# Kernel tuning notes

Hardware: AMD Instinct MI355X
Metric: run time of the kernel (lower is better)

## Reference

```python
import jax, jax.numpy as jnp
import numpy as np

NUM_ENTS = 1000
NUM_RELS = 100
HIDDEN = 200
N_QUERY = 50000
N_HIST = 1000000
ALPHA = 0.5


def setup_inputs() -> dict:
    key = jax.random.key(0)
    ks = jax.random.split(key, 12)
    s = 0.05  # small init for numerical stability (xavier-like scale)
    return {
        "ent_emb": jax.random.normal(ks[0], (NUM_ENTS, HIDDEN), jnp.float32) * s,
        "rel_emb": jax.random.normal(ks[1], (NUM_RELS, HIDDEN), jnp.float32) * s,
        "tim_emb": jax.random.normal(ks[2], (1, HIDDEN), jnp.float32) * s,
        "g_w": jax.random.normal(ks[3], (3 * HIDDEN, HIDDEN), jnp.float32) * s,
        "g_b": jnp.zeros((HIDDEN,), jnp.float32),
        "c_w": jax.random.normal(ks[4], (3 * HIDDEN, HIDDEN), jnp.float32) * s,
        "c_b": jnp.zeros((HIDDEN,), jnp.float32),
        "hist_sub": jax.random.randint(ks[5], (N_HIST,), 0, NUM_ENTS, jnp.int32),
        "hist_rel": jax.random.randint(ks[6], (N_HIST,), 0, NUM_RELS, jnp.int32),
        "hist_obj": jax.random.randint(ks[7], (N_HIST,), 0, NUM_ENTS, jnp.int32),
        "sub": jax.random.randint(ks[8], (N_QUERY,), 0, NUM_ENTS, jnp.int32),
        "rel": jax.random.randint(ks[9], (N_QUERY,), 0, NUM_RELS, jnp.int32),
    }


def reference(ent_emb, rel_emb, tim_emb, g_w, g_b, c_w, c_b,
              hist_sub, hist_rel, hist_obj, sub, rel):
    E = ent_emb.shape[0]
    R = rel_emb.shape[0]
    N = sub.shape[0]
    # Triple-count histogram over all history graphs (fused scatter-add;
    # equivalent to the per-graph python loop vocab[s,r,o] += 1).
    vocab = jnp.zeros((E, R, E), jnp.float32).at[hist_sub, hist_rel, hist_obj].add(1.0)
    # Query features: [N, 3H]
    x = jnp.concatenate(
        [ent_emb[sub], rel_emb[rel], jnp.broadcast_to(tim_emb, (N, tim_emb.shape[1]))],
        axis=1)
    # Generate-mode score distribution
    gscore = jax.nn.softmax(x @ g_w + g_b, axis=1)  # [N, H]
    # Copy-mode mask: 1 where the (sub, rel) pair occurred in history
    mask = (vocab[sub, rel].sum(axis=1, keepdims=True) != 0).astype(x.dtype)  # [N, 1]
    cscore = jax.nn.softmax(jnp.tanh(x @ c_w + c_b) + mask, axis=1)  # [N, H]
    fscore = gscore + ALPHA * (cscore - gscore)
    return jnp.log(fscore)
```

## Files before the change

kernel.cpp:

```cpp
#include <hip/hip_runtime.h>
#include <math.h>

#define HIDDEN 200
#define RPB 8

#define LOG2E 1.4426950408889634f
#define LN2   0.6931471805599453f

typedef float f32x4 __attribute__((ext_vector_type(4)));

__global__ __launch_bounds__(256) void precompute_kernel(
    const float* __restrict__ ent, const float* __restrict__ rel,
    const float* __restrict__ tim,
    const float* __restrict__ g_w, const float* __restrict__ g_b,
    const float* __restrict__ c_w, const float* __restrict__ c_b,
    float* __restrict__ Ag, float* __restrict__ Ac,
    float* __restrict__ Bg, float* __restrict__ Bc) {
  const float* in;
  const float* w;
  const float* bias = nullptr;
  float* out;
  int nrows, k0;
  bool fold_tim = false;
  switch (blockIdx.y) {
    case 0:  in = ent; w = g_w; out = Ag; nrows = 1000; k0 = 0;   break;
    case 1:  in = ent; w = c_w; out = Ac; nrows = 1000; k0 = 0;   break;
    case 2:  in = rel; w = g_w; out = Bg; nrows = 100;  k0 = 200;
             fold_tim = true; bias = g_b; break;
    default: in = rel; w = c_w; out = Bc; nrows = 100;  k0 = 200;
             fold_tim = true; bias = c_b; break;
  }
  int row0 = blockIdx.x * RPB;
  if (row0 >= nrows) return;
  int nr = nrows - row0;
  if (nr > RPB) nr = RPB;

  __shared__ float a_lds[RPB][HIDDEN];
  __shared__ float t_lds[HIDDEN];
  int c = threadIdx.x;
  if (c < HIDDEN) {
    for (int j = 0; j < nr; ++j) a_lds[j][c] = in[(row0 + j) * HIDDEN + c];
    if (fold_tim) t_lds[c] = tim[c];
  }
  __syncthreads();
  if (c >= HIDDEN) return;

  float acc[RPB];
  #pragma unroll
  for (int j = 0; j < RPB; ++j) acc[j] = 0.f;
  const float* wp = w + k0 * HIDDEN + c;
  #pragma unroll 4
  for (int k = 0; k < HIDDEN; ++k) {
    float wv = wp[k * HIDDEN];
    #pragma unroll
    for (int j = 0; j < RPB; ++j) acc[j] += a_lds[j][k] * wv;
  }
  float extra = 0.f;
  if (fold_tim) {
    const float* wt = w + 400 * HIDDEN + c;
    float t = 0.f;
    #pragma unroll 4
    for (int k = 0; k < HIDDEN; ++k) t += t_lds[k] * wt[k * HIDDEN];
    extra = t + bias[c];
  }
  for (int j = 0; j < nr; ++j) out[(row0 + j) * HIDDEN + c] = acc[j] + extra;
}

__global__ __launch_bounds__(256) void query_kernel(
    const float* __restrict__ Ag, const float* __restrict__ Ac,
    const float* __restrict__ Bg, const float* __restrict__ Bc,
    const int* __restrict__ sub, const int* __restrict__ rel,
    float* __restrict__ out, int N) {
  int gtid = blockIdx.x * blockDim.x + threadIdx.x;
  int q = gtid >> 6;
  int lane = threadIdx.x & 63;
  if (q >= N) return;

  int s = __builtin_amdgcn_readfirstlane(sub[q]);
  int r = __builtin_amdgcn_readfirstlane(rel[q]);
  bool act = lane < (HIDDEN / 4);

  float eg[4], ec[4];
  float sg = 0.f, sc = 0.f;
  if (act) {
    float4 a = ((const float4*)(Ag + s * HIDDEN))[lane];
    float4 b = ((const float4*)(Bg + r * HIDDEN))[lane];
    float lg0 = a.x + b.x, lg1 = a.y + b.y, lg2 = a.z + b.z, lg3 = a.w + b.w;
    eg[0] = __builtin_amdgcn_exp2f(lg0 * LOG2E);
    eg[1] = __builtin_amdgcn_exp2f(lg1 * LOG2E);
    eg[2] = __builtin_amdgcn_exp2f(lg2 * LOG2E);
    eg[3] = __builtin_amdgcn_exp2f(lg3 * LOG2E);
    sg = (eg[0] + eg[1]) + (eg[2] + eg[3]);

    a = ((const float4*)(Ac + s * HIDDEN))[lane];
    b = ((const float4*)(Bc + r * HIDDEN))[lane];
    float xc[4] = {a.x + b.x, a.y + b.y, a.z + b.z, a.w + b.w};
    #pragma unroll
    for (int j = 0; j < 4; ++j) {
      float x = fminf(fmaxf(xc[j], -10.f), 10.f);
      float e2 = __builtin_amdgcn_exp2f(x * (2.f * LOG2E));
      float th = (e2 - 1.f) * __builtin_amdgcn_rcpf(e2 + 1.f);
      ec[j] = __builtin_amdgcn_exp2f(th * LOG2E);
      sc += ec[j];
    }
  }
  #pragma unroll
  for (int m = 32; m > 0; m >>= 1) {
    sg += __shfl_xor(sg, m);
    sc += __shfl_xor(sc, m);
  }

  if (act) {
    float ig = 0.5f * __builtin_amdgcn_rcpf(sg);
    float ic = 0.5f * __builtin_amdgcn_rcpf(sc);
    f32x4 o;
    o.x = __builtin_amdgcn_logf(eg[0] * ig + ec[0] * ic) * LN2;
    o.y = __builtin_amdgcn_logf(eg[1] * ig + ec[1] * ic) * LN2;
    o.z = __builtin_amdgcn_logf(eg[2] * ig + ec[2] * ic) * LN2;
    o.w = __builtin_amdgcn_logf(eg[3] * ig + ec[3] * ic) * LN2;
    __builtin_nontemporal_store(o, (f32x4*)(out + q * HIDDEN) + lane);
  }
}

extern "C" void kernel_launch(void* const* d_in, const int* in_sizes, int n_in,
                              void* d_out, int out_size, void* d_ws, size_t ws_size,
                              hipStream_t stream) {
  const float* ent  = (const float*)d_in[0];
  const float* relE = (const float*)d_in[1];
  const float* tim  = (const float*)d_in[2];
  const float* g_w  = (const float*)d_in[3];
  const float* g_b  = (const float*)d_in[4];
  const float* c_w  = (const float*)d_in[5];
  const float* c_b  = (const float*)d_in[6];
  const int* sub = (const int*)d_in[10];
  const int* rel = (const int*)d_in[11];
  float* out = (float*)d_out;
  int N = in_sizes[10];

  float* ws = (float*)d_ws;
  float* Ag = ws;
  float* Ac = ws + 200000;
  float* Bg = ws + 400000;
  float* Bc = ws + 420000;

  dim3 grid1((1000 + RPB - 1) / RPB, 4);
  precompute_kernel<<<grid1, 256, 0, stream>>>(ent, relE, tim, g_w, g_b, c_w,
                                               c_b, Ag, Ac, Bg, Bc);

  long long threads = (long long)N * 64;
  int blocks = (int)((threads + 255) / 256);
  query_kernel<<<blocks, 256, 0, stream>>>(Ag, Ac, Bg, Bc, sub, rel, out, N);
}
```

Before: 138.9 us.

## Precompute exponentiated gen logits, interleave tables, and factor the log-sum

The precompute kernel now stores exp of the generate-mode partial logits, so the query kernel gets the softmax numerator as a product of entity and relation terms instead of an add followed by exp. The g and c tables are interleaved per row so one query reads a single contiguous 400-float row for the entity and one for the relation. The final log is rewritten as log(eg*sc+ec*sg) minus a shared log(2*sg*sc), which replaces the two reciprocals and per-element scaling. The precompute grid is restructured to two rows per block with split accumulators. The tanh input clamp is removed, which risks inf/NaN for large inputs, and exp products without max subtraction could overflow for larger weights.

Measured after the change: 125.2 us, median of 2. 9.8% less time.

```diff
diff --git a/kernel.cpp b/kernel.cpp
--- a/kernel.cpp
+++ b/kernel.cpp
@@ -2,8 +2,6 @@
 #include <math.h>
 
 #define HIDDEN 200
-#define RPB 8
-
 #define LOG2E 1.4426950408889634f
 #define LN2   0.6931471805599453f
 
@@ -14,61 +12,62 @@
     const float* __restrict__ tim,
     const float* __restrict__ g_w, const float* __restrict__ g_b,
     const float* __restrict__ c_w, const float* __restrict__ c_b,
-    float* __restrict__ Ag, float* __restrict__ Ac,
-    float* __restrict__ Bg, float* __restrict__ Bc) {
-  const float* in;
-  const float* w;
-  const float* bias = nullptr;
-  float* out;
-  int nrows, k0;
-  bool fold_tim = false;
-  switch (blockIdx.y) {
-    case 0:  in = ent; w = g_w; out = Ag; nrows = 1000; k0 = 0;   break;
-    case 1:  in = ent; w = c_w; out = Ac; nrows = 1000; k0 = 0;   break;
-    case 2:  in = rel; w = g_w; out = Bg; nrows = 100;  k0 = 200;
-             fold_tim = true; bias = g_b; break;
-    default: in = rel; w = c_w; out = Bc; nrows = 100;  k0 = 200;
-             fold_tim = true; bias = c_b; break;
-  }
-  int row0 = blockIdx.x * RPB;
-  if (row0 >= nrows) return;
-  int nr = nrows - row0;
-  if (nr > RPB) nr = RPB;
+    float* __restrict__ EA, float* __restrict__ EB) {
+  const int mode = blockIdx.y;
+  const float* w = mode ? c_w : g_w;
+  const float* bias = mode ? c_b : g_b;
+  const bool is_ent = blockIdx.x < 500;
+  const int row0 = is_ent ? blockIdx.x * 2 : (blockIdx.x - 500) * 2;
+  const float* in = is_ent ? ent : rel;
+  const int k0 = is_ent ? 0 : 200;
+  float* obase = is_ent ? (EA + row0 * 400 + mode * 200)
+                        : (EB + row0 * 400 + mode * 200);
 
-  __shared__ float a_lds[RPB][HIDDEN];
-  __shared__ float t_lds[HIDDEN];
-  int c = threadIdx.x;
+  __shared__ float a0[HIDDEN], a1[HIDDEN], tl[HIDDEN];
+  const int c = threadIdx.x;
   if (c < HIDDEN) {
-    for (int j = 0; j < nr; ++j) a_lds[j][c] = in[(row0 + j) * HIDDEN + c];
-    if (fold_tim) t_lds[c] = tim[c];
+    a0[c] = in[row0 * HIDDEN + c];
+    a1[c] = in[(row0 + 1) * HIDDEN + c];
+    if (!is_ent) tl[c] = tim[c];
   }
   __syncthreads();
   if (c >= HIDDEN) return;
 
-  float acc[RPB];
-  #pragma unroll
-  for (int j = 0; j < RPB; ++j) acc[j] = 0.f;
   const float* wp = w + k0 * HIDDEN + c;
+  float acc0a = 0.f, acc0b = 0.f, acc1a = 0.f, acc1b = 0.f;
   #pragma unroll 4
-  for (int k = 0; k < HIDDEN; ++k) {
-    float wv = wp[k * HIDDEN];
-    #pragma unroll
-    for (int j = 0; j < RPB; ++j) acc[j] += a_lds[j][k] * wv;
+  for (int k = 0; k < 100; ++k) {
+    float w0 = wp[k * HIDDEN];
+    float w1 = wp[(k + 100) * HIDDEN];
+    acc0a += a0[k] * w0;
+    acc0b += a0[k + 100] * w1;
+    acc1a += a1[k] * w0;
+    acc1b += a1[k + 100] * w1;
   }
-  float extra = 0.f;
-  if (fold_tim) {
+  float r0 = acc0a + acc0b;
+  float r1 = acc1a + acc1b;
+  if (!is_ent) {
     const float* wt = w + 400 * HIDDEN + c;
-    float t = 0.f;
+    float ta = 0.f, tb = 0.f;
     #pragma unroll 4
-    for (int k = 0; k < HIDDEN; ++k) t += t_lds[k] * wt[k * HIDDEN];
-    extra = t + bias[c];
+    for (int k = 0; k < 100; ++k) {
+      ta += tl[k] * wt[k * HIDDEN];
+      tb += tl[k + 100] * wt[(k + 100) * HIDDEN];
+    }
+    float extra = ta + tb + bias[c];
+    r0 += extra;
+    r1 += extra;
   }
-  for (int j = 0; j < nr; ++j) out[(row0 + j) * HIDDEN + c] = acc[j] + extra;
+  if (mode == 0) {
+    r0 = __builtin_amdgcn_exp2f(r0 * LOG2E);
+    r1 = __builtin_amdgcn_exp2f(r1 * LOG2E);
+  }
+  obase[c] = r0;
+  obase[400 + c] = r1;
 }
 
 __global__ __launch_bounds__(256) void query_kernel(
-    const float* __restrict__ Ag, const float* __restrict__ Ac,
-    const float* __restrict__ Bg, const float* __restrict__ Bc,
+    const float* __restrict__ EA, const float* __restrict__ EB,
     const int* __restrict__ sub, const int* __restrict__ rel,
     float* __restrict__ out, int N) {
   int gtid = blockIdx.x * blockDim.x + threadIdx.x;
@@ -80,25 +79,18 @@
   int r = __builtin_amdgcn_readfirstlane(rel[q]);
   bool act = lane < (HIDDEN / 4);
 
-  float eg[4], ec[4];
+  const f32x4* ea = (const f32x4*)(EA + s * 400);
+  const f32x4* eb = (const f32x4*)(EB + r * 400);
+
+  f32x4 eg, ec;
   float sg = 0.f, sc = 0.f;
   if (act) {
-    float4 a = ((const float4*)(Ag + s * HIDDEN))[lane];
-    float4 b = ((const float4*)(Bg + r * HIDDEN))[lane];
-    float lg0 = a.x + b.x, lg1 = a.y + b.y, lg2 = a.z + b.z, lg3 = a.w + b.w;
-    eg[0] = __builtin_amdgcn_exp2f(lg0 * LOG2E);
-    eg[1] = __builtin_amdgcn_exp2f(lg1 * LOG2E);
-    eg[2] = __builtin_amdgcn_exp2f(lg2 * LOG2E);
-    eg[3] = __builtin_amdgcn_exp2f(lg3 * LOG2E);
+    eg = ea[lane] * eb[lane];
     sg = (eg[0] + eg[1]) + (eg[2] + eg[3]);
-
-    a = ((const float4*)(Ac + s * HIDDEN))[lane];
-    b = ((const float4*)(Bc + r * HIDDEN))[lane];
-    float xc[4] = {a.x + b.x, a.y + b.y, a.z + b.z, a.w + b.w};
+    f32x4 xc = ea[lane + 50] + eb[lane + 50];
     #pragma unroll
     for (int j = 0; j < 4; ++j) {
-      float x = fminf(fmaxf(xc[j], -10.f), 10.f);
-      float e2 = __builtin_amdgcn_exp2f(x * (2.f * LOG2E));
+      float e2 = __builtin_amdgcn_exp2f(xc[j] * (2.f * LOG2E));
       float th = (e2 - 1.f) * __builtin_amdgcn_rcpf(e2 + 1.f);
       ec[j] = __builtin_amdgcn_exp2f(th * LOG2E);
       sc += ec[j];
@@ -111,13 +103,13 @@
   }
 
   if (act) {
-    float ig = 0.5f * __builtin_amdgcn_rcpf(sg);
-    float ic = 0.5f * __builtin_amdgcn_rcpf(sc);
+    float kl = __builtin_amdgcn_logf(2.f * sg * sc) * LN2;
     f32x4 o;
-    o.x = __builtin_amdgcn_logf(eg[0] * ig + ec[0] * ic) * LN2;
-    o.y = __builtin_amdgcn_logf(eg[1] * ig + ec[1] * ic) * LN2;
-    o.z = __builtin_amdgcn_logf(eg[2] * ig + ec[2] * ic) * LN2;
-    o.w = __builtin_amdgcn_logf(eg[3] * ig + ec[3] * ic) * LN2;
+    #pragma unroll
+    for (int j = 0; j < 4; ++j) {
+      float num = eg[j] * sc + ec[j] * sg;
+      o[j] = fmaf(__builtin_amdgcn_logf(num), LN2, -kl);
+    }
     __builtin_nontemporal_store(o, (f32x4*)(out + q * HIDDEN) + lane);
   }
 }
@@ -138,16 +130,14 @@
   int N = in_sizes[10];
 
   float* ws = (float*)d_ws;
-  float* Ag = ws;
-  float* Ac = ws + 200000;
-  float* Bg = ws + 400000;
-  float* Bc = ws + 420000;
+  float* EA = ws;
+  float* EB = ws + 400000;
 
-  dim3 grid1((1000 + RPB - 1) / RPB, 4);
+  dim3 grid1(550, 2);
   precompute_kernel<<<grid1, 256, 0, stream>>>(ent, relE, tim, g_w, g_b, c_w,
-                                               c_b, Ag, Ac, Bg, Bc);
+                                               c_b, EA, EB);
 
   long long threads = (long long)N * 64;
   int blocks = (int)((threads + 255) / 256);
-  query_kernel<<<blocks, 256, 0, stream>>>(Ag, Ac, Bg, Bc, sub, rel, out, N);
+  query_kernel<<<blocks, 256, 0, stream>>>(EA, EB, sub, rel, out, N);
 }
```
